# Kernel optimization log

Measured on AMD Instinct MI355X. Metric: run time of the kernel, lower is better.

The kernel has to match this reference:

```python
import jax, jax.numpy as jnp
import numpy as np

HID, QK_NOPE, QK_ROPE, Q_LR, KV_LR, H, V_DIM = 2048, 128, 64, 768, 512, 16, 128
QK_HEAD = QK_NOPE + QK_ROPE
THETA = 10000.0
EPS = 1e-5


def _layernorm(x, g, b):
    mu = jnp.mean(x, axis=-1, keepdims=True)
    var = jnp.mean(jnp.square(x - mu), axis=-1, keepdims=True)
    return (x - mu) * jax.lax.rsqrt(var + EPS) * g + b


def _rotate_half(x):
    x1, x2 = jnp.split(x, 2, axis=-1)
    return jnp.concatenate([-x2, x1], axis=-1)


def setup_inputs() -> dict:
    key = jax.random.key(0)
    ks = jax.random.split(key, 6)
    s = 0.02
    return {
        "hidden_state": jax.random.normal(ks[0], (2, 4096, HID), dtype=jnp.float32),
        "w_qa": jax.random.normal(ks[1], (Q_LR, HID), dtype=jnp.float32) * s,
        "b_qa": jnp.zeros((Q_LR,), jnp.float32),
        "g_qa_ln": jnp.ones((Q_LR,), jnp.float32),
        "b_qa_ln": jnp.zeros((Q_LR,), jnp.float32),
        "w_qb": jax.random.normal(ks[2], (H * QK_HEAD, Q_LR), dtype=jnp.float32) * s,
        "b_qb": jnp.zeros((H * QK_HEAD,), jnp.float32),
        "w_kva": jax.random.normal(ks[3], (KV_LR + QK_ROPE, HID), dtype=jnp.float32) * s,
        "b_kva": jnp.zeros((KV_LR + QK_ROPE,), jnp.float32),
        "g_kva_ln": jnp.ones((KV_LR,), jnp.float32),
        "b_kva_ln": jnp.zeros((KV_LR,), jnp.float32),
        "w_kvb": jax.random.normal(ks[4], (H * (QK_NOPE + V_DIM), KV_LR), dtype=jnp.float32) * s,
        "b_kvb": jnp.zeros((H * (QK_NOPE + V_DIM),), jnp.float32),
    }


def reference(hidden_state, w_qa, b_qa, g_qa_ln, b_qa_ln, w_qb, b_qb,
              w_kva, b_kva, g_kva_ln, b_kva_ln, w_kvb, b_kvb):
    B, S, _ = hidden_state.shape
    # ----- Q path: low-rank down-proj -> LN -> up-proj -----
    q_c = hidden_state @ w_qa.T + b_qa                      # [B,S,Q_LR]
    q_c = _layernorm(q_c, g_qa_ln, b_qa_ln)
    q = (q_c @ w_qb.T + b_qb).reshape(B, S, H, QK_HEAD).transpose(0, 2, 1, 3)  # [B,H,S,QK_HEAD]
    q_nope, q_rope = q[..., :QK_NOPE], q[..., QK_NOPE:]
    # ----- KV path -----
    kv_c = hidden_state @ w_kva.T + b_kva                   # [B,S,KV_LR+ROPE]
    kv_lr, k_rope = kv_c[..., :KV_LR], kv_c[..., KV_LR:]
    kv_lr = _layernorm(kv_lr, g_kva_ln, b_kva_ln)
    kv = (kv_lr @ w_kvb.T + b_kvb).reshape(B, S, H, QK_NOPE + V_DIM).transpose(0, 2, 1, 3)
    k_nope, v = kv[..., :QK_NOPE], kv[..., QK_NOPE:]
    # ----- RoPE on the rope slice only -----
    inv_freq = 1.0 / THETA ** (jnp.arange(0, QK_ROPE, 2, dtype=jnp.float32) / QK_ROPE)
    freq = jnp.arange(S, dtype=jnp.float32)[:, None] * inv_freq[None, :]   # [S, ROPE/2]
    cos = jnp.concatenate([jnp.cos(freq), jnp.cos(freq)], axis=-1)[None, None]  # [1,1,S,ROPE]
    sin = jnp.concatenate([jnp.sin(freq), jnp.sin(freq)], axis=-1)[None, None]
    k_rope = k_rope[:, None]                                # [B,1,S,ROPE]
    q_rot = q_rope * cos + _rotate_half(q_rope) * sin       # [B,H,S,ROPE]
    k_rot = k_rope * cos + _rotate_half(k_rope) * sin       # [B,1,S,ROPE]
    k_rot = jnp.broadcast_to(k_rot, (B, H, S, QK_ROPE))
    q_full = jnp.concatenate([q_nope, q_rot], axis=-1)      # [B,H,S,QK_HEAD]
    k_full = jnp.concatenate([k_nope, k_rot], axis=-1)      # [B,H,S,QK_HEAD]
    # original forward stops after building q,k,v; return them concatenated
    return jnp.concatenate([q_full, k_full, v], axis=-1)    # [B,H,S,2*QK_HEAD+V_DIM]
```

## Files before the change

### kernel.cpp

```cpp
#include <hip/hip_runtime.h>

typedef unsigned short u16;
typedef __bf16 bf16x8 __attribute__((ext_vector_type(8)));
typedef float f32x4 __attribute__((ext_vector_type(4)));


__device__ __forceinline__ u16 f2bf(float f) {
  unsigned u = __float_as_uint(f);
  u += 0x7fffu + ((u >> 16) & 1u);
  return (u16)(u >> 16);
}

__device__ __forceinline__ void load_lds16(const void* g, void* l) {
  __builtin_amdgcn_global_load_lds(
      (const __attribute__((address_space(1))) void*)g,
      (__attribute__((address_space(3))) void*)l, 16, 0, 0);
}


__device__ __forceinline__ void conv_seg(const float* __restrict__ s,
                                         u16* __restrict__ d, int n4,
                                         int g, int stride) {
  const float4* s4 = (const float4*)s;
  ushort4* d4 = (ushort4*)d;
  for (int i = g; i < n4; i += stride) {
    float4 v = s4[i];
    d4[i] = make_ushort4(f2bf(v.x), f2bf(v.y), f2bf(v.z), f2bf(v.w));
  }
}

__global__ __launch_bounds__(256) void convert_all(
    const float* __restrict__ hid, const float* __restrict__ wqa,
    const float* __restrict__ wqb, const float* __restrict__ wkva,
    const float* __restrict__ wkvb,
    u16* __restrict__ hid_b, u16* __restrict__ wqa_b, u16* __restrict__ wqb_b,
    u16* __restrict__ wkva_b, u16* __restrict__ wkvb_b) {
  int g = blockIdx.x * 256 + threadIdx.x;
  int stride = gridDim.x * 256;
  conv_seg(hid,  hid_b,  16777216 / 4, g, stride);
  conv_seg(wqa,  wqa_b,   1572864 / 4, g, stride);
  conv_seg(wqb,  wqb_b,   2359296 / 4, g, stride);
  conv_seg(wkva, wkva_b,  1179648 / 4, g, stride);
  conv_seg(wkvb, wkvb_b,  2097152 / 4, g, stride);
}


__global__ __launch_bounds__(256) void rope_table(float* __restrict__ cosT,
                                                  float* __restrict__ sinT) {
  int idx = blockIdx.x * 256 + threadIdx.x;
  int s = idx >> 5, i = idx & 31;
  float inv = powf(10000.f, -(float)i / 32.f);
  float f = (float)s * inv;
  float sv, cv;
  sincosf(f, &sv, &cv);
  cosT[idx] = cv;
  sinT[idx] = sv;
}


template <int MODE>
__global__ __launch_bounds__(256, 2) void gemm_bt(
    const u16* __restrict__ A, const u16* __restrict__ B,
    const float* __restrict__ bias, float* __restrict__ Cout, int N, int K,
    const float* __restrict__ cosT, const float* __restrict__ sinT) {
  __shared__ __align__(16) u16 sA[128 * 64];
  __shared__ __align__(16) u16 sB[128 * 64];
  const int tid = threadIdx.x;
  const int lane = tid & 63;
  const int wave = tid >> 6;
  const int wm = (wave >> 1) * 64;
  const int wn = (wave & 1) * 64;
  const int mTile = blockIdx.x * 128;
  const int nTile = blockIdx.y * 128;
  const int lane15 = lane & 15;
  const int quad = lane >> 4;

  f32x4 acc[4][4] = {};

  const int nStages = K >> 6;
  for (int ks = 0; ks < nStages; ++ks) {
    const int k0 = ks << 6;
    if (ks) __syncthreads();
#pragma unroll
    for (int i = 0; i < 4; ++i) {
      int nu = i * 256 + tid;
      int r = nu >> 3, up = nu & 7;
      int ul = up ^ (r & 7);
      const u16* g = A + (size_t)(mTile + r) * K + (k0 + ul * 8);
      load_lds16(g, &sA[(i * 256 + (wave << 6)) * 8]);
    }
#pragma unroll
    for (int i = 0; i < 4; ++i) {
      int nu = i * 256 + tid;
      int r = nu >> 3, up = nu & 7;
      int ul = up ^ (r & 7);
      int row = nTile + r;
      if (row >= N) row = N - 1;
      const u16* g = B + (size_t)row * K + (k0 + ul * 8);
      load_lds16(g, &sB[(i * 256 + (wave << 6)) * 8]);
    }
    __syncthreads();
#pragma unroll
    for (int kk = 0; kk < 2; ++kk) {
      bf16x8 af[4], bfv[4];
#pragma unroll
      for (int mi = 0; mi < 4; ++mi) {
        int r = wm + mi * 16 + lane15;
        int up = (kk * 4 + quad) ^ (r & 7);
        af[mi] = *(const bf16x8*)&sA[(r * 8 + up) * 8];
      }
#pragma unroll
      for (int ni = 0; ni < 4; ++ni) {
        int r = wn + ni * 16 + lane15;
        int up = (kk * 4 + quad) ^ (r & 7);
        bfv[ni] = *(const bf16x8*)&sB[(r * 8 + up) * 8];
      }
#pragma unroll
      for (int mi = 0; mi < 4; ++mi)
#pragma unroll
        for (int ni = 0; ni < 4; ++ni)
          acc[mi][ni] = __builtin_amdgcn_mfma_f32_16x16x32_bf16(
              af[mi], bfv[ni], acc[mi][ni], 0, 0, 0);
    }
  }

  float bv[4];
#pragma unroll
  for (int ni = 0; ni < 4; ++ni) {
    int col = nTile + wn + ni * 16 + lane15;
    bv[ni] = (col < N) ? bias[col] : 0.f;
  }

  if (MODE == 0) {
#pragma unroll
    for (int mi = 0; mi < 4; ++mi)
#pragma unroll
      for (int reg = 0; reg < 4; ++reg) {
        int row = mTile + wm + mi * 16 + quad * 4 + reg;
#pragma unroll
        for (int ni = 0; ni < 4; ++ni) {
          int col = nTile + wn + ni * 16 + lane15;
          if (col < N) Cout[(size_t)row * N + col] = acc[mi][ni][reg] + bv[ni];
        }
      }
  } else if (MODE == 1) {
    const int colW = nTile + wn;
    const int h = colW / 192;
    const int jBase = colW % 192;
    if (jBase != 128) {
#pragma unroll
      for (int mi = 0; mi < 4; ++mi)
#pragma unroll
        for (int reg = 0; reg < 4; ++reg) {
          int row = mTile + wm + mi * 16 + quad * 4 + reg;
          int bb = row >> 12, ss = row & 4095;
          size_t ob = ((size_t)((bb * 16 + h) * 4096 + ss)) * 512 + jBase;
#pragma unroll
          for (int ni = 0; ni < 4; ++ni)
            Cout[ob + ni * 16 + lane15] = acc[mi][ni][reg] + bv[ni];
        }
    } else {
#pragma unroll
      for (int ni = 0; ni < 2; ++ni) {
        int i = ni * 16 + lane15;
#pragma unroll
        for (int mi = 0; mi < 4; ++mi)
#pragma unroll
          for (int reg = 0; reg < 4; ++reg) {
            int row = mTile + wm + mi * 16 + quad * 4 + reg;
            int bb = row >> 12, ss = row & 4095;
            float cv = cosT[ss * 32 + i], sv = sinT[ss * 32 + i];
            float x1 = acc[mi][ni][reg] + bv[ni];
            float x2 = acc[mi][ni + 2][reg] + bv[ni + 2];
            size_t ob = ((size_t)((bb * 16 + h) * 4096 + ss)) * 512 + 128;
            Cout[ob + i] = x1 * cv - x2 * sv;
            Cout[ob + 32 + i] = x2 * cv + x1 * sv;
          }
      }
    }
  } else {
    const int colW = nTile + wn;
    const int h = colW >> 8;
    const int jBase = colW & 255;
    const int chBase = (jBase < 128) ? (192 + jBase) : (256 + jBase);
#pragma unroll
    for (int mi = 0; mi < 4; ++mi)
#pragma unroll
      for (int reg = 0; reg < 4; ++reg) {
        int row = mTile + wm + mi * 16 + quad * 4 + reg;
        int bb = row >> 12, ss = row & 4095;
        size_t ob = ((size_t)((bb * 16 + h) * 4096 + ss)) * 512 + chBase;
#pragma unroll
        for (int ni = 0; ni < 4; ++ni)
          Cout[ob + ni * 16 + lane15] = acc[mi][ni][reg] + bv[ni];
      }
  }
}


__device__ __forceinline__ void reduce2(float& s1, float& s2, float* rs,
                                        float* rq) {
#pragma unroll
  for (int off = 32; off > 0; off >>= 1) {
    s1 += __shfl_down(s1, off, 64);
    s2 += __shfl_down(s2, off, 64);
  }
  int lane = threadIdx.x & 63, wave = threadIdx.x >> 6;
  if (lane == 0) { rs[wave] = s1; rq[wave] = s2; }
  __syncthreads();
  s1 = rs[0] + rs[1] + rs[2] + rs[3];
  s2 = rq[0] + rq[1] + rq[2] + rq[3];
  __syncthreads();
}

__global__ __launch_bounds__(256) void ln_rot(
    const float* __restrict__ qc, const float* __restrict__ kvc,
    const float* __restrict__ g_q, const float* __restrict__ b_q,
    const float* __restrict__ g_kv, const float* __restrict__ b_kv,
    u16* __restrict__ q_ln, u16* __restrict__ kv_ln,
    const float* __restrict__ cosT, const float* __restrict__ sinT,
    float* __restrict__ out) {
  __shared__ float rs[4], rq[4];
  __shared__ float rot[64];
  const int t = blockIdx.x;
  const int tid = threadIdx.x;
  const int bb = t >> 12, ss = t & 4095;

  {
    const float* p = qc + (size_t)t * 768;
    float v[3], sum = 0.f, sq = 0.f;
#pragma unroll
    for (int j = 0; j < 3; ++j) {
      v[j] = p[tid + j * 256];
      sum += v[j];
      sq += v[j] * v[j];
    }
    reduce2(sum, sq, rs, rq);
    float mu = sum * (1.f / 768.f);
    float var = sq * (1.f / 768.f) - mu * mu;
    float inv = rsqrtf(var + 1e-5f);
#pragma unroll
    for (int j = 0; j < 3; ++j) {
      int c = tid + j * 256;
      q_ln[(size_t)t * 768 + c] = f2bf((v[j] - mu) * inv * g_q[c] + b_q[c]);
    }
  }
  {
    const float* p = kvc + (size_t)t * 576;
    float v[2], sum = 0.f, sq = 0.f;
#pragma unroll
    for (int j = 0; j < 2; ++j) {
      v[j] = p[tid + j * 256];
      sum += v[j];
      sq += v[j] * v[j];
    }
    reduce2(sum, sq, rs, rq);
    float mu = sum * (1.f / 512.f);
    float var = sq * (1.f / 512.f) - mu * mu;
    float inv = rsqrtf(var + 1e-5f);
#pragma unroll
    for (int j = 0; j < 2; ++j) {
      int c = tid + j * 256;
      kv_ln[(size_t)t * 512 + c] = f2bf((v[j] - mu) * inv * g_kv[c] + b_kv[c]);
    }
  }
  if (tid < 32) {
    const float* p = kvc + (size_t)t * 576 + 512;
    float k1 = p[tid], k2 = p[tid + 32];
    float cv = cosT[ss * 32 + tid], sv = sinT[ss * 32 + tid];
    rot[tid] = k1 * cv - k2 * sv;
    rot[tid + 32] = k2 * cv + k1 * sv;
  }
  __syncthreads();
  for (int u = tid; u < 1024; u += 256) {
    int h = u >> 6, i2 = u & 63;
    out[((size_t)((bb * 16 + h) * 4096 + ss)) * 512 + 320 + i2] = rot[i2];
  }
}


extern "C" void kernel_launch(void* const* d_in, const int* in_sizes, int n_in,
                              void* d_out, int out_size, void* d_ws,
                              size_t ws_size, hipStream_t stream) {
  const float* hidden = (const float*)d_in[0];
  const float* w_qa = (const float*)d_in[1];
  const float* b_qa = (const float*)d_in[2];
  const float* g_qa_ln = (const float*)d_in[3];
  const float* b_qa_ln = (const float*)d_in[4];
  const float* w_qb = (const float*)d_in[5];
  const float* b_qb = (const float*)d_in[6];
  const float* w_kva = (const float*)d_in[7];
  const float* b_kva = (const float*)d_in[8];
  const float* g_kva_ln = (const float*)d_in[9];
  const float* b_kva_ln = (const float*)d_in[10];
  const float* w_kvb = (const float*)d_in[11];
  const float* b_kvb = (const float*)d_in[12];
  float* out = (float*)d_out;

  char* ws = (char*)d_ws;
  u16* hid_bf = (u16*)ws;            ws += (size_t)16777216 * 2;
  u16* wqa_bf = (u16*)ws;            ws += (size_t)1572864 * 2;
  u16* wqb_bf = (u16*)ws;            ws += (size_t)2359296 * 2;
  u16* wkva_bf = (u16*)ws;           ws += (size_t)1179648 * 2;
  u16* wkvb_bf = (u16*)ws;           ws += (size_t)2097152 * 2;
  float* qc = (float*)ws;            ws += (size_t)6291456 * 4;
  float* kvc = (float*)ws;           ws += (size_t)4718592 * 4;
  u16* q_ln = (u16*)ws;              ws += (size_t)6291456 * 2;
  u16* kv_ln = (u16*)ws;             ws += (size_t)4194304 * 2;
  float* cosT = (float*)ws;          ws += (size_t)131072 * 4;
  float* sinT = (float*)ws;          ws += (size_t)131072 * 4;

  convert_all<<<dim3(1024), dim3(256), 0, stream>>>(
      hidden, w_qa, w_qb, w_kva, w_kvb, hid_bf, wqa_bf, wqb_bf, wkva_bf,
      wkvb_bf);
  rope_table<<<dim3(512), dim3(256), 0, stream>>>(cosT, sinT);
  gemm_bt<0><<<dim3(64, 6), dim3(256), 0, stream>>>(hid_bf, wqa_bf, b_qa, qc,
                                                    768, 2048, cosT, sinT);
  gemm_bt<0><<<dim3(64, 5), dim3(256), 0, stream>>>(hid_bf, wkva_bf, b_kva,
                                                    kvc, 576, 2048, cosT, sinT);
  ln_rot<<<dim3(8192), dim3(256), 0, stream>>>(qc, kvc, g_qa_ln, b_qa_ln,
                                               g_kva_ln, b_kva_ln, q_ln, kv_ln,
                                               cosT, sinT, out);
  gemm_bt<1><<<dim3(64, 24), dim3(256), 0, stream>>>(q_ln, wqb_bf, b_qb, out,
                                                     3072, 768, cosT, sinT);
  gemm_bt<2><<<dim3(64, 32), dim3(256), 0, stream>>>(kv_ln, wkvb_bf, b_kvb, out,
                                                     4096, 512, cosT, sinT);
}
```

Measured before the change: 535.5 us.

## Merge down-projection and up-projection GEMMs, stage epilogue through LDS for vector stores

Concatenates w_qa and w_kva into one weight so a single GEMM produces a fused qkvc buffer, and merges the two up-projection GEMMs into one launch that dispatches by blockIdx.y. The prep kernel absorbs the rope table computation and builds the combined bias. GEMM epilogues are rewritten to transpose accumulator fragments through swizzled LDS so each lane writes float4 rows instead of scattered scalar stores, and ln_rot writes its rope slice with float4 stores. The aim is fewer launches, less reloading of hidden_state, and coalesced output writes, at the cost of an extra LDS round trip and extra barriers in the epilogue.

```diff
diff --git a/kernel.cpp b/kernel.cpp
--- a/kernel.cpp
+++ b/kernel.cpp
@@ -16,7 +16,6 @@
       (const __attribute__((address_space(1))) void*)g,
       (__attribute__((address_space(3))) void*)l, 16, 0, 0);
 }
-
 
 __device__ __forceinline__ void conv_seg(const float* __restrict__ s,
                                          u16* __restrict__ d, int n4,
@@ -29,51 +28,68 @@
   }
 }
 
-__global__ __launch_bounds__(256) void convert_all(
+
+__global__ __launch_bounds__(256) void prep(
     const float* __restrict__ hid, const float* __restrict__ wqa,
-    const float* __restrict__ wqb, const float* __restrict__ wkva,
-    const float* __restrict__ wkvb,
-    u16* __restrict__ hid_b, u16* __restrict__ wqa_b, u16* __restrict__ wqb_b,
-    u16* __restrict__ wkva_b, u16* __restrict__ wkvb_b) {
+    const float* __restrict__ wkva, const float* __restrict__ wqb,
+    const float* __restrict__ wkvb, const float* __restrict__ bqa,
+    const float* __restrict__ bkva, u16* __restrict__ hid_b,
+    u16* __restrict__ wab_b, u16* __restrict__ wqb_b,
+    u16* __restrict__ wkvb_b, float* __restrict__ bias_ab,
+    float* __restrict__ cosT, float* __restrict__ sinT) {
   int g = blockIdx.x * 256 + threadIdx.x;
   int stride = gridDim.x * 256;
-  conv_seg(hid,  hid_b,  16777216 / 4, g, stride);
-  conv_seg(wqa,  wqa_b,   1572864 / 4, g, stride);
-  conv_seg(wqb,  wqb_b,   2359296 / 4, g, stride);
-  conv_seg(wkva, wkva_b,  1179648 / 4, g, stride);
-  conv_seg(wkvb, wkvb_b,  2097152 / 4, g, stride);
-}
-
-
-__global__ __launch_bounds__(256) void rope_table(float* __restrict__ cosT,
-                                                  float* __restrict__ sinT) {
-  int idx = blockIdx.x * 256 + threadIdx.x;
-  int s = idx >> 5, i = idx & 31;
-  float inv = powf(10000.f, -(float)i / 32.f);
-  float f = (float)s * inv;
-  float sv, cv;
-  sincosf(f, &sv, &cv);
-  cosT[idx] = cv;
-  sinT[idx] = sv;
-}
-
-
-template <int MODE>
-__global__ __launch_bounds__(256, 2) void gemm_bt(
-    const u16* __restrict__ A, const u16* __restrict__ B,
-    const float* __restrict__ bias, float* __restrict__ Cout, int N, int K,
-    const float* __restrict__ cosT, const float* __restrict__ sinT) {
-  __shared__ __align__(16) u16 sA[128 * 64];
-  __shared__ __align__(16) u16 sB[128 * 64];
+  conv_seg(hid, hid_b, 4194304, g, stride);
+  conv_seg(wqa, wab_b, 393216, g, stride);
+  conv_seg(wkva, wab_b + 768 * 2048, 294912, g, stride);
+  conv_seg(wqb, wqb_b, 589824, g, stride);
+  conv_seg(wkvb, wkvb_b, 524288, g, stride);
+  if (g < 1344) bias_ab[g] = (g < 768) ? bqa[g] : bkva[g - 768];
+  for (int idx = g; idx < 131072; idx += stride) {
+    int s = idx >> 5, i = idx & 31;
+    float inv = powf(10000.f, -(float)i / 32.f);
+    float f = (float)s * inv;
+    float sv, cv;
+    sincosf(f, &sv, &cv);
+    cosT[idx] = cv;
+    sinT[idx] = sv;
+  }
+}
+
+
+template <int WHICH>
+__global__ __launch_bounds__(256, 2) void gemm_k(
+    const u16* __restrict__ A0, const u16* __restrict__ B0,
+    const float* __restrict__ bias0, float* __restrict__ C0,
+    const u16* __restrict__ qA, const u16* __restrict__ qB,
+    const float* __restrict__ qb, const u16* __restrict__ kA,
+    const u16* __restrict__ kB, const float* __restrict__ kb,
+    float* __restrict__ out, const float* __restrict__ cosT,
+    const float* __restrict__ sinT) {
+  __shared__ __align__(16) u16 smem[2 * 128 * 64];
+  u16* sA = smem;
+  u16* sB = smem + 128 * 64;
   const int tid = threadIdx.x;
   const int lane = tid & 63;
   const int wave = tid >> 6;
   const int wm = (wave >> 1) * 64;
   const int wn = (wave & 1) * 64;
-  const int mTile = blockIdx.x * 128;
-  const int nTile = blockIdx.y * 128;
   const int lane15 = lane & 15;
   const int quad = lane >> 4;
+  const int mTile = blockIdx.x * 128;
+
+  const u16* A;
+  const u16* B;
+  const float* bias;
+  int K, nTile, mode;
+  if (WHICH == 0) {
+    A = A0; B = B0; bias = bias0; K = 2048; nTile = blockIdx.y * 128; mode = 0;
+  } else if (blockIdx.y < 24) {
+    A = qA; B = qB; bias = qb; K = 768; nTile = blockIdx.y * 128; mode = 1;
+  } else {
+    A = kA; B = kB; bias = kb; K = 512; nTile = (blockIdx.y - 24) * 128;
+    mode = 2;
+  }
 
   f32x4 acc[4][4] = {};
 
@@ -84,20 +100,20 @@
 #pragma unroll
     for (int i = 0; i < 4; ++i) {
       int nu = i * 256 + tid;
-      int r = nu >> 3, up = nu & 7;
-      int ul = up ^ (r & 7);
-      const u16* g = A + (size_t)(mTile + r) * K + (k0 + ul * 8);
-      load_lds16(g, &sA[(i * 256 + (wave << 6)) * 8]);
+      int rr = nu >> 3, u = nu & 7;
+      int ul = u ^ (rr & 7);
+      load_lds16(A + (size_t)(mTile + rr) * K + (k0 + ul * 8),
+                 &sA[(i * 256 + (wave << 6)) * 8]);
     }
 #pragma unroll
     for (int i = 0; i < 4; ++i) {
       int nu = i * 256 + tid;
-      int r = nu >> 3, up = nu & 7;
-      int ul = up ^ (r & 7);
-      int row = nTile + r;
-      if (row >= N) row = N - 1;
-      const u16* g = B + (size_t)row * K + (k0 + ul * 8);
-      load_lds16(g, &sB[(i * 256 + (wave << 6)) * 8]);
+      int rr = nu >> 3, u = nu & 7;
+      int ul = u ^ (rr & 7);
+      int brow = nTile + rr;
+      if (WHICH == 0 && brow >= 1344) brow = 1343;
+      load_lds16(B + (size_t)brow * K + (k0 + ul * 8),
+                 &sB[(i * 256 + (wave << 6)) * 8]);
     }
     __syncthreads();
 #pragma unroll
@@ -106,14 +122,14 @@
 #pragma unroll
       for (int mi = 0; mi < 4; ++mi) {
         int r = wm + mi * 16 + lane15;
-        int up = (kk * 4 + quad) ^ (r & 7);
-        af[mi] = *(const bf16x8*)&sA[(r * 8 + up) * 8];
+        int u = (kk * 4 + quad) ^ (r & 7);
+        af[mi] = *(const bf16x8*)&sA[(r * 8 + u) * 8];
       }
 #pragma unroll
       for (int ni = 0; ni < 4; ++ni) {
         int r = wn + ni * 16 + lane15;
-        int up = (kk * 4 + quad) ^ (r & 7);
-        bfv[ni] = *(const bf16x8*)&sB[(r * 8 + up) * 8];
+        int u = (kk * 4 + quad) ^ (r & 7);
+        bfv[ni] = *(const bf16x8*)&sB[(r * 8 + u) * 8];
       }
 #pragma unroll
       for (int mi = 0; mi < 4; ++mi)
@@ -124,76 +140,81 @@
     }
   }
 
+  const int colW = nTile + wn;
   float bv[4];
 #pragma unroll
   for (int ni = 0; ni < 4; ++ni) {
-    int col = nTile + wn + ni * 16 + lane15;
-    bv[ni] = (col < N) ? bias[col] : 0.f;
-  }
-
-  if (MODE == 0) {
-#pragma unroll
-    for (int mi = 0; mi < 4; ++mi)
-#pragma unroll
-      for (int reg = 0; reg < 4; ++reg) {
-        int row = mTile + wm + mi * 16 + quad * 4 + reg;
-#pragma unroll
-        for (int ni = 0; ni < 4; ++ni) {
-          int col = nTile + wn + ni * 16 + lane15;
-          if (col < N) Cout[(size_t)row * N + col] = acc[mi][ni][reg] + bv[ni];
+    int col = colW + ni * 16 + lane15;
+    if (WHICH == 0)
+      bv[ni] = (col < 1344) ? bias[col] : 0.f;
+    else
+      bv[ni] = bias[col];
+  }
+
+  int h = 0, ch0 = 0;
+  if (mode == 1) {
+    h = colW / 192;
+    ch0 = colW % 192;
+  } else if (mode == 2) {
+    int jb = colW & 255;
+    h = colW >> 8;
+    ch0 = (jb < 128) ? (192 + jb) : (256 + jb);
+  }
+  const bool ropeTile = (mode == 1) && (ch0 == 128);
+
+  __syncthreads();
+  float* lw = (float*)smem + wave * (16 * 68);
+  const int hi = lane15 >> 2, l3 = lane15 & 3;
+
+#pragma unroll
+  for (int mi = 0; mi < 4; ++mi) {
+    f32x4 v[4];
+#pragma unroll
+    for (int ni = 0; ni < 4; ++ni)
+#pragma unroll
+      for (int rg = 0; rg < 4; ++rg) v[ni][rg] = acc[mi][ni][rg] + bv[ni];
+
+    if (ropeTile) {
+      int rowB = mTile + wm + mi * 16 + quad * 4;
+#pragma unroll
+      for (int rg = 0; rg < 4; ++rg) {
+        int ss = (rowB + rg) & 4095;
+#pragma unroll
+        for (int ni = 0; ni < 2; ++ni) {
+          int i = ni * 16 + lane15;
+          float cv = cosT[ss * 32 + i], sv = sinT[ss * 32 + i];
+          float x1 = v[ni][rg], x2 = v[ni + 2][rg];
+          v[ni][rg] = x1 * cv - x2 * sv;
+          v[ni + 2][rg] = x2 * cv + x1 * sv;
         }
       }
-  } else if (MODE == 1) {
-    const int colW = nTile + wn;
-    const int h = colW / 192;
-    const int jBase = colW % 192;
-    if (jBase != 128) {
-#pragma unroll
-      for (int mi = 0; mi < 4; ++mi)
-#pragma unroll
-        for (int reg = 0; reg < 4; ++reg) {
-          int row = mTile + wm + mi * 16 + quad * 4 + reg;
-          int bb = row >> 12, ss = row & 4095;
-          size_t ob = ((size_t)((bb * 16 + h) * 4096 + ss)) * 512 + jBase;
-#pragma unroll
-          for (int ni = 0; ni < 4; ++ni)
-            Cout[ob + ni * 16 + lane15] = acc[mi][ni][reg] + bv[ni];
-        }
-    } else {
-#pragma unroll
-      for (int ni = 0; ni < 2; ++ni) {
-        int i = ni * 16 + lane15;
-#pragma unroll
-        for (int mi = 0; mi < 4; ++mi)
-#pragma unroll
-          for (int reg = 0; reg < 4; ++reg) {
-            int row = mTile + wm + mi * 16 + quad * 4 + reg;
-            int bb = row >> 12, ss = row & 4095;
-            float cv = cosT[ss * 32 + i], sv = sinT[ss * 32 + i];
-            float x1 = acc[mi][ni][reg] + bv[ni];
-            float x2 = acc[mi][ni + 2][reg] + bv[ni + 2];
-            size_t ob = ((size_t)((bb * 16 + h) * 4096 + ss)) * 512 + 128;
-            Cout[ob + i] = x1 * cv - x2 * sv;
-            Cout[ob + 32 + i] = x2 * cv + x1 * sv;
-          }
+    }
+
+    if (mi) asm volatile("s_waitcnt lgkmcnt(0)" ::: "memory");
+#pragma unroll
+    for (int ni = 0; ni < 4; ++ni) {
+      int su = (4 * ni + hi) ^ quad;
+#pragma unroll
+      for (int rg = 0; rg < 4; ++rg)
+        lw[68 * (quad * 4 + rg) + 4 * su + l3] = v[ni][rg];
+    }
+    asm volatile("s_waitcnt lgkmcnt(0)" ::: "memory");
+#pragma unroll
+    for (int j = 0; j < 4; ++j) {
+      int rr = 4 * j + quad;
+      int su = lane15 ^ j;
+      float4 o = *(const float4*)&lw[68 * rr + 4 * su];
+      int row = mTile + wm + mi * 16 + rr;
+      if (mode == 0) {
+        if (colW + 4 * lane15 < 1344)
+          *(float4*)(C0 + (size_t)row * 1344 + colW + 4 * lane15) = o;
+      } else {
+        int bb = row >> 12, ss = row & 4095;
+        size_t ob =
+            ((size_t)((bb * 16 + h) * 4096 + ss)) * 512 + ch0 + 4 * lane15;
+        *(float4*)(out + ob) = o;
       }
     }
-  } else {
-    const int colW = nTile + wn;
-    const int h = colW >> 8;
-    const int jBase = colW & 255;
-    const int chBase = (jBase < 128) ? (192 + jBase) : (256 + jBase);
-#pragma unroll
-    for (int mi = 0; mi < 4; ++mi)
-#pragma unroll
-      for (int reg = 0; reg < 4; ++reg) {
-        int row = mTile + wm + mi * 16 + quad * 4 + reg;
-        int bb = row >> 12, ss = row & 4095;
-        size_t ob = ((size_t)((bb * 16 + h) * 4096 + ss)) * 512 + chBase;
-#pragma unroll
-        for (int ni = 0; ni < 4; ++ni)
-          Cout[ob + ni * 16 + lane15] = acc[mi][ni][reg] + bv[ni];
-      }
   }
 }
 
@@ -214,20 +235,19 @@
 }
 
 __global__ __launch_bounds__(256) void ln_rot(
-    const float* __restrict__ qc, const float* __restrict__ kvc,
-    const float* __restrict__ g_q, const float* __restrict__ b_q,
-    const float* __restrict__ g_kv, const float* __restrict__ b_kv,
-    u16* __restrict__ q_ln, u16* __restrict__ kv_ln,
-    const float* __restrict__ cosT, const float* __restrict__ sinT,
-    float* __restrict__ out) {
+    const float* __restrict__ qkvc, const float* __restrict__ g_q,
+    const float* __restrict__ b_q, const float* __restrict__ g_kv,
+    const float* __restrict__ b_kv, u16* __restrict__ q_ln,
+    u16* __restrict__ kv_ln, const float* __restrict__ cosT,
+    const float* __restrict__ sinT, float* __restrict__ out) {
   __shared__ float rs[4], rq[4];
-  __shared__ float rot[64];
+  __shared__ __align__(16) float rot[64];
   const int t = blockIdx.x;
   const int tid = threadIdx.x;
   const int bb = t >> 12, ss = t & 4095;
+  const float* p = qkvc + (size_t)t * 1344;
 
   {
-    const float* p = qc + (size_t)t * 768;
     float v[3], sum = 0.f, sq = 0.f;
 #pragma unroll
     for (int j = 0; j < 3; ++j) {
@@ -246,11 +266,10 @@
     }
   }
   {
-    const float* p = kvc + (size_t)t * 576;
     float v[2], sum = 0.f, sq = 0.f;
 #pragma unroll
     for (int j = 0; j < 2; ++j) {
-      v[j] = p[tid + j * 256];
+      v[j] = p[768 + tid + j * 256];
       sum += v[j];
       sq += v[j] * v[j];
     }
@@ -265,16 +284,17 @@
     }
   }
   if (tid < 32) {
-    const float* p = kvc + (size_t)t * 576 + 512;
-    float k1 = p[tid], k2 = p[tid + 32];
+    float k1 = p[1280 + tid], k2 = p[1312 + tid];
     float cv = cosT[ss * 32 + tid], sv = sinT[ss * 32 + tid];
     rot[tid] = k1 * cv - k2 * sv;
     rot[tid + 32] = k2 * cv + k1 * sv;
   }
   __syncthreads();
-  for (int u = tid; u < 1024; u += 256) {
-    int h = u >> 6, i2 = u & 63;
-    out[((size_t)((bb * 16 + h) * 4096 + ss)) * 512 + 320 + i2] = rot[i2];
+  {
+    int hh = tid >> 4, c4 = tid & 15;
+    float4 o = ((const float4*)rot)[c4];
+    *(float4*)(out + ((size_t)((bb * 16 + hh) * 4096 + ss)) * 512 + 320 +
+               4 * c4) = o;
   }
 }
 
@@ -298,31 +318,27 @@
   float* out = (float*)d_out;
 
   char* ws = (char*)d_ws;
-  u16* hid_bf = (u16*)ws;            ws += (size_t)16777216 * 2;
-  u16* wqa_bf = (u16*)ws;            ws += (size_t)1572864 * 2;
-  u16* wqb_bf = (u16*)ws;            ws += (size_t)2359296 * 2;
-  u16* wkva_bf = (u16*)ws;           ws += (size_t)1179648 * 2;
-  u16* wkvb_bf = (u16*)ws;           ws += (size_t)2097152 * 2;
-  float* qc = (float*)ws;            ws += (size_t)6291456 * 4;
-  float* kvc = (float*)ws;           ws += (size_t)4718592 * 4;
-  u16* q_ln = (u16*)ws;              ws += (size_t)6291456 * 2;
-  u16* kv_ln = (u16*)ws;             ws += (size_t)4194304 * 2;
-  float* cosT = (float*)ws;          ws += (size_t)131072 * 4;
-  float* sinT = (float*)ws;          ws += (size_t)131072 * 4;
-
-  convert_all<<<dim3(1024), dim3(256), 0, stream>>>(
-      hidden, w_qa, w_qb, w_kva, w_kvb, hid_bf, wqa_bf, wqb_bf, wkva_bf,
-      wkvb_bf);
-  rope_table<<<dim3(512), dim3(256), 0, stream>>>(cosT, sinT);
-  gemm_bt<0><<<dim3(64, 6), dim3(256), 0, stream>>>(hid_bf, wqa_bf, b_qa, qc,
-                                                    768, 2048, cosT, sinT);
-  gemm_bt<0><<<dim3(64, 5), dim3(256), 0, stream>>>(hid_bf, wkva_bf, b_kva,
-                                                    kvc, 576, 2048, cosT, sinT);
-  ln_rot<<<dim3(8192), dim3(256), 0, stream>>>(qc, kvc, g_qa_ln, b_qa_ln,
+  u16* hid_bf = (u16*)ws;   ws += (size_t)16777216 * 2;
+  u16* wab_bf = (u16*)ws;   ws += (size_t)1344 * 2048 * 2;
+  u16* wqb_bf = (u16*)ws;   ws += (size_t)2359296 * 2;
+  u16* wkvb_bf = (u16*)ws;  ws += (size_t)2097152 * 2;
+  float* qkvc = (float*)ws; ws += (size_t)8192 * 1344 * 4;
+  u16* q_ln = (u16*)ws;     ws += (size_t)6291456 * 2;
+  u16* kv_ln = (u16*)ws;    ws += (size_t)4194304 * 2;
+  float* cosT = (float*)ws; ws += (size_t)131072 * 4;
+  float* sinT = (float*)ws; ws += (size_t)131072 * 4;
+  float* bias_ab = (float*)ws; ws += (size_t)2048 * 4;
+
+  prep<<<dim3(1024), dim3(256), 0, stream>>>(
+      hidden, w_qa, w_kva, w_qb, w_kvb, b_qa, b_kva, hid_bf, wab_bf, wqb_bf,
+      wkvb_bf, bias_ab, cosT, sinT);
+  gemm_k<0><<<dim3(64, 11), dim3(256), 0, stream>>>(
+      hid_bf, wab_bf, bias_ab, qkvc, nullptr, nullptr, nullptr, nullptr,
+      nullptr, nullptr, nullptr, cosT, sinT);
+  ln_rot<<<dim3(8192), dim3(256), 0, stream>>>(qkvc, g_qa_ln, b_qa_ln,
                                                g_kva_ln, b_kva_ln, q_ln, kv_ln,
                                                cosT, sinT, out);
-  gemm_bt<1><<<dim3(64, 24), dim3(256), 0, stream>>>(q_ln, wqb_bf, b_qb, out,
-                                                     3072, 768, cosT, sinT);
-  gemm_bt<2><<<dim3(64, 32), dim3(256), 0, stream>>>(kv_ln, wkvb_bf, b_kvb, out,
-                                                     4096, 512, cosT, sinT);
-}
+  gemm_k<1><<<dim3(64, 56), dim3(256), 0, stream>>>(
+      nullptr, nullptr, nullptr, nullptr, q_ln, wqb_bf, b_qb, kv_ln, wkvb_bf,
+      b_kvb, out, cosT, sinT);
+}
```

Result: faster. 473.7 us (-11.5%).
